# Kernel tuning notes

Hardware: AMD Instinct MI355X
Metric: run time of the kernel (lower is better)

## Reference

```python
import jax, jax.numpy as jnp
import numpy as np
import math

D, H, DK, F, V, L = 512, 8, 64, 2048, 8192, 2
B, S, T = 16, 128, 128
EPS = 1e-5


def _ln(x, g, b):
    mu = jnp.mean(x, -1, keepdims=True)
    var = jnp.mean((x - mu) ** 2, -1, keepdims=True)
    return g * (x - mu) * jax.lax.rsqrt(var + EPS) + b


def _pe(length):
    pos = jnp.arange(length, dtype=jnp.float32)[:, None]
    div = jnp.exp(jnp.arange(0, D, 2, dtype=jnp.float32) * (-math.log(10000.0) / D))
    ang = pos * div
    pe = jnp.zeros((length, D), jnp.float32)
    return pe.at[:, 0::2].set(jnp.sin(ang)).at[:, 1::2].set(jnp.cos(ang))


def _attn(q, k, v, src, dst, num_dst):
    # per-edge score = exp(clip((k_src . q_dst)/sqrt(d_k), -5, 5))  [E, H]
    score = jnp.einsum('ehd,ehd->eh', k[src], q[dst]) / math.sqrt(DK)
    score = jnp.exp(jnp.clip(score, -5.0, 5.0))
    wv = jax.ops.segment_sum(v[src] * score[..., None], dst, num_segments=num_dst)
    z = jax.ops.segment_sum(score, dst, num_segments=num_dst)
    return (wv / z[..., None]).reshape(num_dst, D)


def _forward(src_tokens, tgt_tokens, ee_src, ee_dst, dd_src, dd_dst, ed_src, ed_dst, P):
    (src_emb, tgt_emb, eW, eB, elg, elb, eW1, eb1, eW2, eb2, eng, enb,
     dsW, dsB, dcW, dcB, dlg, dlb, dW1, db1, dW2, db2, dng, dnb, gW, gb) = P
    pe = _pe(max(S, T))
    Ne, Nd = B * S, B * T
    xe = (src_emb[src_tokens] * math.sqrt(D) + pe[None, :S]).reshape(Ne, D)
    xd = (tgt_emb[tgt_tokens] * math.sqrt(D) + pe[None, :T]).reshape(Nd, D)
    # encoder stack
    for i in range(L):
        nx = _ln(xe, elg[i, 0], elb[i, 0])
        q = (nx @ eW[i, 0] + eB[i, 0]).reshape(Ne, H, DK)
        k = (nx @ eW[i, 1] + eB[i, 1]).reshape(Ne, H, DK)
        v = (nx @ eW[i, 2] + eB[i, 2]).reshape(Ne, H, DK)
        xe = xe + _attn(q, k, v, ee_src, ee_dst, Ne) @ eW[i, 3] + eB[i, 3]
        nx = _ln(xe, elg[i, 1], elb[i, 1])
        xe = xe + jax.nn.relu(nx @ eW1[i] + eb1[i]) @ eW2[i] + eb2[i]
        if i == L - 1:
            xe = _ln(xe, eng, enb)
    # decoder stack
    for i in range(L):
        nx = _ln(xd, dlg[i, 0], dlb[i, 0])
        q = (nx @ dsW[i, 0] + dsB[i, 0]).reshape(Nd, H, DK)
        k = (nx @ dsW[i, 1] + dsB[i, 1]).reshape(Nd, H, DK)
        v = (nx @ dsW[i, 2] + dsB[i, 2]).reshape(Nd, H, DK)
        xd = xd + _attn(q, k, v, dd_src, dd_dst, Nd) @ dsW[i, 3] + dsB[i, 3]
        nq = _ln(xd, dlg[i, 1], dlb[i, 1])
        nkv = _ln(xe, dlg[i, 1], dlb[i, 1])
        q = (nq @ dcW[i, 0] + dcB[i, 0]).reshape(Nd, H, DK)
        k = (nkv @ dcW[i, 1] + dcB[i, 1]).reshape(Ne, H, DK)
        v = (nkv @ dcW[i, 2] + dcB[i, 2]).reshape(Ne, H, DK)
        xd = xd + _attn(q, k, v, ed_src, ed_dst, Nd) @ dcW[i, 3] + dcB[i, 3]
        nx = _ln(xd, dlg[i, 2], dlb[i, 2])
        xd = xd + jax.nn.relu(nx @ dW1[i] + db1[i]) @ dW2[i] + db2[i]
        if i == L - 1:
            xd = _ln(xd, dng, dnb)
    return jax.nn.log_softmax(xd @ gW + gb, axis=-1)  # [Nd, V]


def setup_inputs() -> dict:
    key = jax.random.key(0)
    ks = iter(jax.random.split(key, 40))
    def nrm(shape, scale=0.02):
        return jax.random.normal(next(ks), shape, dtype=jnp.float32) * scale
    src_tokens = jax.random.randint(next(ks), (B, S), 0, V, dtype=jnp.int32)
    tgt_tokens = jax.random.randint(next(ks), (B, T), 0, V, dtype=jnp.int32)
    # graph structure (per-sentence blocks)
    si, di = np.meshgrid(np.arange(S), np.arange(S), indexing='ij')
    si, di = si.ravel(), di.ravel()
    base = (np.arange(B) * S)[:, None]
    ee_src = (base + si[None, :]).ravel().astype(np.int32)
    ee_dst = (base + di[None, :]).ravel().astype(np.int32)
    m = si <= di  # causal: src pos <= dst pos
    dd_src = (base + si[m][None, :]).ravel().astype(np.int32)
    dd_dst = (base + di[m][None, :]).ravel().astype(np.int32)
    ed_src = ee_src.copy()
    ed_dst = ee_dst.copy()
    inp = dict(
        src_tokens=src_tokens, tgt_tokens=tgt_tokens,
        ee_src=jnp.asarray(ee_src), ee_dst=jnp.asarray(ee_dst),
        dd_src=jnp.asarray(dd_src), dd_dst=jnp.asarray(dd_dst),
        ed_src=jnp.asarray(ed_src), ed_dst=jnp.asarray(ed_dst),
        src_emb=nrm((V, D), 1.0 / math.sqrt(D)), tgt_emb=nrm((V, D), 1.0 / math.sqrt(D)),
        enc_attn_W=nrm((L, 4, D, D)), enc_attn_b=jnp.zeros((L, 4, D), jnp.float32),
        enc_ln_g=jnp.ones((L, 2, D), jnp.float32), enc_ln_b=jnp.zeros((L, 2, D), jnp.float32),
        enc_ff_W1=nrm((L, D, F)), enc_ff_b1=jnp.zeros((L, F), jnp.float32),
        enc_ff_W2=nrm((L, F, D)), enc_ff_b2=jnp.zeros((L, D), jnp.float32),
        enc_norm_g=jnp.ones((D,), jnp.float32), enc_norm_b=jnp.zeros((D,), jnp.float32),
        dec_self_W=nrm((L, 4, D, D)), dec_self_b=jnp.zeros((L, 4, D), jnp.float32),
        dec_cross_W=nrm((L, 4, D, D)), dec_cross_b=jnp.zeros((L, 4, D), jnp.float32),
        dec_ln_g=jnp.ones((L, 3, D), jnp.float32), dec_ln_b=jnp.zeros((L, 3, D), jnp.float32),
        dec_ff_W1=nrm((L, D, F)), dec_ff_b1=jnp.zeros((L, F), jnp.float32),
        dec_ff_W2=nrm((L, F, D)), dec_ff_b2=jnp.zeros((L, D), jnp.float32),
        dec_norm_g=jnp.ones((D,), jnp.float32), dec_norm_b=jnp.zeros((D,), jnp.float32),
        gen_W=nrm((D, V)), gen_b=jnp.zeros((V,), jnp.float32),
    )
    return inp


def reference(src_tokens, tgt_tokens, ee_src, ee_dst, dd_src, dd_dst, ed_src, ed_dst,
              src_emb, tgt_emb, enc_attn_W, enc_attn_b, enc_ln_g, enc_ln_b,
              enc_ff_W1, enc_ff_b1, enc_ff_W2, enc_ff_b2, enc_norm_g, enc_norm_b,
              dec_self_W, dec_self_b, dec_cross_W, dec_cross_b, dec_ln_g, dec_ln_b,
              dec_ff_W1, dec_ff_b1, dec_ff_W2, dec_ff_b2, dec_norm_g, dec_norm_b,
              gen_W, gen_b):
    P = (src_emb, tgt_emb, enc_attn_W, enc_attn_b, enc_ln_g, enc_ln_b,
         enc_ff_W1, enc_ff_b1, enc_ff_W2, enc_ff_b2, enc_norm_g, enc_norm_b,
         dec_self_W, dec_self_b, dec_cross_W, dec_cross_b, dec_ln_g, dec_ln_b,
         dec_ff_W1, dec_ff_b1, dec_ff_W2, dec_ff_b2, dec_norm_g, dec_norm_b, gen_W, gen_b)
    return _forward(src_tokens, tgt_tokens, ee_src, ee_dst, dd_src, dd_dst, ed_src, ed_dst, P)
```

## Files before the change

### kernel.cpp

```cpp
#include <hip/hip_runtime.h>

typedef __attribute__((ext_vector_type(8))) short bfx8;
typedef __attribute__((ext_vector_type(4))) float fx4;

static __device__ __forceinline__ unsigned short f2bf(float f) {
    union { float f; unsigned int u; } v; v.f = f;
    unsigned int i = v.u;
    return (unsigned short)((i + 0x7FFFu + ((i >> 16) & 1u)) >> 16);
}
static __device__ __forceinline__ float bf2f(unsigned short u) {
    union { unsigned int ui; float f; } cv;
    cv.ui = ((unsigned int)u) << 16;
    return cv.f;
}

static __device__ __forceinline__ void gl2lds16(const unsigned short* g, unsigned short* l) {
    unsigned long long gu = (unsigned long long)g;
    unsigned int lu = (unsigned int)(unsigned long long)l;
    __builtin_amdgcn_global_load_lds(
        (const __attribute__((address_space(1))) void*)gu,
        (__attribute__((address_space(3))) void*)lu,
        16, 0, 0);
}

struct TrGroup {
    const float* src;
    unsigned short* dst;
    int srcRowStride;
    int dstRowStride;
    long srcSliceOff;
    long dstSliceOff;
};
struct TrTable {
    TrGroup g[18];
    int zStart[19];
};

__global__ __launch_bounds__(256) void trall_kernel(TrTable tt)
{
    __shared__ unsigned short tile[32][33];
    int z = blockIdx.z;
    int gi = 0;
#pragma unroll 1
    while (z >= tt.zStart[gi + 1]) ++gi;
    int zi = z - tt.zStart[gi];
    const float* s = tt.g[gi].src + (size_t)zi * tt.g[gi].srcSliceOff;
    unsigned short* d = tt.g[gi].dst + (size_t)zi * tt.g[gi].dstSliceOff;
    int srs = tt.g[gi].srcRowStride, drs = tt.g[gi].dstRowStride;
    int n0 = blockIdx.x * 32, k0 = blockIdx.y * 32;
    int tx = threadIdx.x & 31, ty = threadIdx.x >> 5;
#pragma unroll
    for (int i = 0; i < 32; i += 8)
        tile[ty + i][tx] = f2bf(s[(size_t)(k0 + ty + i) * srs + (n0 + tx)]);
    __syncthreads();
#pragma unroll
    for (int i = 0; i < 32; i += 8)
        d[(size_t)(n0 + ty + i) * drs + (k0 + tx)] = tile[tx][ty + i];
}

__global__ __launch_bounds__(256) void embed2_kernel(
    const int* __restrict__ tokA, const int* __restrict__ tokB,
    const float* __restrict__ embA, const float* __restrict__ embB,
    float* __restrict__ outA, float* __restrict__ outB)
{
    int idx = blockIdx.x;
    int row = idx & 2047;
    const int* tok = idx < 2048 ? tokA : tokB;
    const float* emb = idx < 2048 ? embA : embB;
    float* out = idx < 2048 ? outA : outB;
    int pos = row & 127;
    int t = tok[row];
    for (int d = threadIdx.x; d < 512; d += 256) {
        float ang = (float)pos * expf((float)(d & ~1) * (-9.210340371976184f / 512.0f));
        float pe = (d & 1) ? cosf(ang) : sinf(ang);
        out[(size_t)row * 512 + d] = emb[(size_t)t * 512 + d] * 22.627416997969522f + pe;
    }
}

static __device__ __forceinline__ void ln_row(
    const float* __restrict__ xrow, const float* __restrict__ g,
    const float* __restrict__ b, int lane, fx4& o0, fx4& o1)
{
    const fx4* xr = (const fx4*)xrow;
    fx4 a = xr[lane * 2], c = xr[lane * 2 + 1];
    float s = a[0] + a[1] + a[2] + a[3] + c[0] + c[1] + c[2] + c[3];
#pragma unroll
    for (int off = 32; off; off >>= 1) s += __shfl_xor(s, off);
    float mu = s * (1.0f / 512.0f);
    float qv = 0.f;
#pragma unroll
    for (int j = 0; j < 4; ++j) {
        float d0 = a[j] - mu; qv += d0 * d0;
        float d1 = c[j] - mu; qv += d1 * d1;
    }
#pragma unroll
    for (int off = 32; off; off >>= 1) qv += __shfl_xor(qv, off);
    float rs = rsqrtf(qv * (1.0f / 512.0f) + 1e-5f);
    const fx4* gr = (const fx4*)g;
    const fx4* br = (const fx4*)b;
    fx4 g0 = gr[lane * 2], g1 = gr[lane * 2 + 1];
    fx4 b0 = br[lane * 2], b1 = br[lane * 2 + 1];
#pragma unroll
    for (int j = 0; j < 4; ++j) {
        o0[j] = g0[j] * (a[j] - mu) * rs + b0[j];
        o1[j] = g1[j] * (c[j] - mu) * rs + b1[j];
    }
}

template<bool OUTBF>
__global__ __launch_bounds__(256) void ln_kernel(
    const float* __restrict__ x, const float* __restrict__ g,
    const float* __restrict__ b, void* __restrict__ out)
{
    int row = blockIdx.x * 4 + (threadIdx.x >> 6);
    int lane = threadIdx.x & 63;
    fx4 o0, o1;
    ln_row(x + (size_t)row * 512, g, b, lane, o0, o1);
    if (OUTBF) {
        unsigned short* orow = (unsigned short*)out + (size_t)row * 512 + lane * 8;
        ushort4 u0 = {f2bf(o0[0]), f2bf(o0[1]), f2bf(o0[2]), f2bf(o0[3])};
        ushort4 u1 = {f2bf(o1[0]), f2bf(o1[1]), f2bf(o1[2]), f2bf(o1[3])};
        *(ushort4*)orow = u0;
        *(ushort4*)(orow + 4) = u1;
    } else {
        fx4* orow = (fx4*)out + (size_t)row * 128;
        orow[lane * 2] = o0;
        orow[lane * 2 + 1] = o1;
    }
}

__global__ __launch_bounds__(256) void ln2_kernel(
    const float* __restrict__ x0, const float* __restrict__ x1,
    const float* __restrict__ g, const float* __restrict__ b,
    unsigned short* __restrict__ o0, unsigned short* __restrict__ o1)
{
    int idx = blockIdx.x * 4 + (threadIdx.x >> 6);
    int lane = threadIdx.x & 63;
    const float* x = idx < 2048 ? x0 : x1;
    unsigned short* o = idx < 2048 ? o0 : o1;
    int row = idx & 2047;
    fx4 v0, v1;
    ln_row(x + (size_t)row * 512, g, b, lane, v0, v1);
    unsigned short* orow = o + (size_t)row * 512 + lane * 8;
    ushort4 u0 = {f2bf(v0[0]), f2bf(v0[1]), f2bf(v0[2]), f2bf(v0[3])};
    ushort4 u1 = {f2bf(v1[0]), f2bf(v1[1]), f2bf(v1[2]), f2bf(v1[3])};
    *(ushort4*)orow = u0;
    *(ushort4*)(orow + 4) = u1;
}

template<bool RELU, bool RESID, bool OUTBF>
__global__ __launch_bounds__(256) void gemm_kernel(
    const unsigned short* __restrict__ A, const unsigned short* __restrict__ Wt,
    const float* __restrict__ bias, const float* __restrict__ res,
    void* __restrict__ Cv, int K, int ldc, int gx)
{
    __shared__ unsigned short smem[2][2][4096];
    const int tid = threadIdx.x;
    const int nwg = gridDim.x;
    const int cpx = nwg >> 3;
    const int phys = blockIdx.x;
    const int logical = (phys & 7) * cpx + (phys >> 3);
    const int bm = (logical / gx) * 64;
    const int bn = (logical % gx) * 64;
    const int lane = tid & 63;
    const int wv = tid >> 6;
    const int wr = (wv >> 1) * 32;
    const int wc = (wv & 1) * 32;
    const int lr = lane & 15;
    const int lrow = lane >> 3;
    const int lchk = lane & 7;
    fx4 acc00 = {0.f, 0.f, 0.f, 0.f}, acc01 = {0.f, 0.f, 0.f, 0.f};
    fx4 acc10 = {0.f, 0.f, 0.f, 0.f}, acc11 = {0.f, 0.f, 0.f, 0.f};

    auto stage = [&](int buf, int k0) {
#pragma unroll
        for (int j = 0; j < 2; ++j) {
            int row = wv * 16 + j * 8 + lrow;
            int sc = lchk ^ (row & 7);
            gl2lds16(A + (size_t)(bm + row) * K + k0 + sc * 8,
                     &smem[buf][0][(wv * 16 + j * 8) * 64]);
        }
#pragma unroll
        for (int j = 0; j < 2; ++j) {
            int row = wv * 16 + j * 8 + lrow;
            int sc = lchk ^ (row & 7);
            gl2lds16(Wt + (size_t)(bn + row) * K + k0 + sc * 8,
                     &smem[buf][1][(wv * 16 + j * 8) * 64]);
        }
    };

    const int nt = K >> 6;
    int cur = 0;
    stage(0, 0);
    for (int t = 0; t < nt; ++t) {
        __syncthreads();
        if (t + 1 < nt) stage(cur ^ 1, (t + 1) << 6);
        const unsigned short* bufA = &smem[cur][0][0];
        const unsigned short* bufB = &smem[cur][1][0];
        const int ra0 = wr + lr, ra1 = wr + 16 + lr;
        const int rb0 = wc + lr, rb1 = wc + 16 + lr;
#pragma unroll
        for (int kk = 0; kk < 2; ++kk) {
            int ca = kk * 4 + (lane >> 4);
            bfx8 a0 = *(const bfx8*)&bufA[ra0 * 64 + ((ca ^ (ra0 & 7)) * 8)];
            bfx8 a1 = *(const bfx8*)&bufA[ra1 * 64 + ((ca ^ (ra1 & 7)) * 8)];
            bfx8 b0 = *(const bfx8*)&bufB[rb0 * 64 + ((ca ^ (rb0 & 7)) * 8)];
            bfx8 b1 = *(const bfx8*)&bufB[rb1 * 64 + ((ca ^ (rb1 & 7)) * 8)];
            acc00 = __builtin_amdgcn_mfma_f32_16x16x32_bf16(a0, b0, acc00, 0, 0, 0);
            acc01 = __builtin_amdgcn_mfma_f32_16x16x32_bf16(a0, b1, acc01, 0, 0, 0);
            acc10 = __builtin_amdgcn_mfma_f32_16x16x32_bf16(a1, b0, acc10, 0, 0, 0);
            acc11 = __builtin_amdgcn_mfma_f32_16x16x32_bf16(a1, b1, acc11, 0, 0, 0);
        }
        cur ^= 1;
    }
    int rbase = bm + wr + ((lane >> 4) * 4);
    int cbase = bn + wc + lr;
#pragma unroll
    for (int m = 0; m < 2; ++m) {
        fx4 am0 = m ? acc10 : acc00;
        fx4 am1 = m ? acc11 : acc01;
#pragma unroll
        for (int r = 0; r < 4; ++r) {
            int row = rbase + m * 16 + r;
#pragma unroll
            for (int half = 0; half < 2; ++half) {
                int col = cbase + half * 16;
                float v = (half ? am1[r] : am0[r]) + bias[col];
                if (RESID) v += res[(size_t)row * ldc + col];
                if (RELU) v = fmaxf(v, 0.f);
                if (OUTBF) ((unsigned short*)Cv)[(size_t)row * ldc + col] = f2bf(v);
                else       ((float*)Cv)[(size_t)row * ldc + col] = v;
            }
        }
    }
}

template<bool RELU, bool RESID, bool OUTBF>
__global__ __launch_bounds__(256) void gemm_bk128_kernel(
    const unsigned short* __restrict__ A, const unsigned short* __restrict__ Wt,
    const float* __restrict__ bias, const float* __restrict__ res,
    void* __restrict__ Cv, int K, int ldc, int gx)
{
    __shared__ unsigned short smem[2][2][8192];
    const int tid = threadIdx.x;
    const int nwg = gridDim.x;
    const int cpx = nwg >> 3;
    const int phys = blockIdx.x;
    const int logical = (phys & 7) * cpx + (phys >> 3);
    const int bm = (logical / gx) * 64;
    const int bn = (logical % gx) * 64;
    const int lane = tid & 63;
    const int wv = tid >> 6;
    const int wr = (wv >> 1) * 32;
    const int wc = (wv & 1) * 32;
    const int lr = lane & 15;
    const int lrow4 = lane >> 4;
    const int lchk16 = lane & 15;
    fx4 acc00 = {0.f, 0.f, 0.f, 0.f}, acc01 = {0.f, 0.f, 0.f, 0.f};
    fx4 acc10 = {0.f, 0.f, 0.f, 0.f}, acc11 = {0.f, 0.f, 0.f, 0.f};

    auto stage = [&](int buf, int k0) {
#pragma unroll
        for (int j = 0; j < 4; ++j) {
            int row = wv * 16 + j * 4 + lrow4;
            int sc = (lchk16 ^ (row & 15)) * 8;
            gl2lds16(A + (size_t)(bm + row) * K + k0 + sc,
                     &smem[buf][0][(wv * 16 + j * 4) * 128]);
            gl2lds16(Wt + (size_t)(bn + row) * K + k0 + sc,
                     &smem[buf][1][(wv * 16 + j * 4) * 128]);
        }
    };

    const int nt = K >> 7;
    int cur = 0;
    stage(0, 0);
    for (int t = 0; t < nt; ++t) {
        __syncthreads();
        if (t + 1 < nt) stage(cur ^ 1, (t + 1) << 7);
        const unsigned short* bufA = &smem[cur][0][0];
        const unsigned short* bufB = &smem[cur][1][0];
        const int ra0 = wr + lr, ra1 = wr + 16 + lr;
        const int rb0 = wc + lr, rb1 = wc + 16 + lr;
#pragma unroll
        for (int kk = 0; kk < 4; ++kk) {
            int ca = kk * 4 + (lane >> 4);
            bfx8 a0 = *(const bfx8*)&bufA[ra0 * 128 + ((ca ^ (ra0 & 15)) * 8)];
            bfx8 a1 = *(const bfx8*)&bufA[ra1 * 128 + ((ca ^ (ra1 & 15)) * 8)];
            bfx8 b0 = *(const bfx8*)&bufB[rb0 * 128 + ((ca ^ (rb0 & 15)) * 8)];
            bfx8 b1 = *(const bfx8*)&bufB[rb1 * 128 + ((ca ^ (rb1 & 15)) * 8)];
            acc00 = __builtin_amdgcn_mfma_f32_16x16x32_bf16(a0, b0, acc00, 0, 0, 0);
            acc01 = __builtin_amdgcn_mfma_f32_16x16x32_bf16(a0, b1, acc01, 0, 0, 0);
            acc10 = __builtin_amdgcn_mfma_f32_16x16x32_bf16(a1, b0, acc10, 0, 0, 0);
            acc11 = __builtin_amdgcn_mfma_f32_16x16x32_bf16(a1, b1, acc11, 0, 0, 0);
        }
        cur ^= 1;
    }
    int rbase = bm + wr + ((lane >> 4) * 4);
    int cbase = bn + wc + lr;
#pragma unroll
    for (int m = 0; m < 2; ++m) {
        fx4 am0 = m ? acc10 : acc00;
        fx4 am1 = m ? acc11 : acc01;
#pragma unroll
        for (int r = 0; r < 4; ++r) {
            int row = rbase + m * 16 + r;
#pragma unroll
            for (int half = 0; half < 2; ++half) {
                int col = cbase + half * 16;
                float v = (half ? am1[r] : am0[r]) + bias[col];
                if (RESID) v += res[(size_t)row * ldc + col];
                if (RELU) v = fmaxf(v, 0.f);
                if (OUTBF) ((unsigned short*)Cv)[(size_t)row * ldc + col] = f2bf(v);
                else       ((float*)Cv)[(size_t)row * ldc + col] = v;
            }
        }
    }
}

template<bool RELU>
__global__ __launch_bounds__(256) void gemm128_kernel(
    const unsigned short* __restrict__ A, const unsigned short* __restrict__ Wt,
    const float* __restrict__ bias, unsigned short* __restrict__ C,
    int K, int ldc)
{
    __shared__ unsigned short smem[2][2][8192];
    const int tid = threadIdx.x;
    const int nwg = gridDim.x;
    const int cpx = nwg >> 3;
    const int phys = blockIdx.x;
    const int logical = (phys & 7) * cpx + (phys >> 3);
    const int bm = (logical & 15) * 128;
    const int bn = (logical >> 4) * 128;
    const int lane = tid & 63;
    const int wv = tid >> 6;
    const int wr = (wv >> 1) * 64;
    const int wc = (wv & 1) * 64;
    const int lr = lane & 15;
    const int lrow = lane >> 3;
    const int lchk = lane & 7;
    fx4 acc[4][4];
#pragma unroll
    for (int mi = 0; mi < 4; ++mi)
#pragma unroll
        for (int ni = 0; ni < 4; ++ni) acc[mi][ni] = fx4{0.f, 0.f, 0.f, 0.f};

    auto stage = [&](int buf, int k0) {
#pragma unroll
        for (int j = 0; j < 4; ++j) {
            int row = wv * 32 + j * 8 + lrow;
            int sc = lchk ^ (row & 7);
            gl2lds16(A + (size_t)(bm + row) * K + k0 + sc * 8,
                     &smem[buf][0][(wv * 32 + j * 8) * 64]);
            gl2lds16(Wt + (size_t)(bn + row) * K + k0 + sc * 8,
                     &smem[buf][1][(wv * 32 + j * 8) * 64]);
        }
    };

    const int nt = K >> 6;
    int cur = 0;
    stage(0, 0);
    for (int t = 0; t < nt; ++t) {
        __syncthreads();
        if (t + 1 < nt) stage(cur ^ 1, (t + 1) << 6);
        const unsigned short* bufA = &smem[cur][0][0];
        const unsigned short* bufB = &smem[cur][1][0];
#pragma unroll
        for (int kk = 0; kk < 2; ++kk) {
            int ca = kk * 4 + (lane >> 4);
            bfx8 af[4], bg[4];
#pragma unroll
            for (int i = 0; i < 4; ++i) {
                int ra = wr + i * 16 + lr;
                int rb = wc + i * 16 + lr;
                af[i] = *(const bfx8*)&bufA[ra * 64 + ((ca ^ (ra & 7)) * 8)];
                bg[i] = *(const bfx8*)&bufB[rb * 64 + ((ca ^ (rb & 7)) * 8)];
            }
#pragma unroll
            for (int mi = 0; mi < 4; ++mi)
#pragma unroll
                for (int ni = 0; ni < 4; ++ni)
                    acc[mi][ni] = __builtin_amdgcn_mfma_f32_16x16x32_bf16(af[mi], bg[ni], acc[mi][ni], 0, 0, 0);
        }
        cur ^= 1;
    }
    int rbase = bm + wr + ((lane >> 4) * 4);
    int cbase = bn + wc + lr;
#pragma unroll
    for (int mi = 0; mi < 4; ++mi)
#pragma unroll
        for (int ni = 0; ni < 4; ++ni) {
            int col = cbase + ni * 16;
            float bv = bias[col];
#pragma unroll
            for (int r = 0; r < 4; ++r) {
                int row = rbase + mi * 16 + r;
                float v = acc[mi][ni][r] + bv;
                if (RELU) v = fmaxf(v, 0.f);
                C[(size_t)row * ldc + col] = f2bf(v);
            }
        }
}

template<bool CAUSAL>
__global__ __launch_bounds__(512) void fattn_kernel(
    const unsigned short* __restrict__ xq, const unsigned short* __restrict__ xkv,
    const unsigned short* __restrict__ Wt, const float* __restrict__ bias,
    unsigned short* __restrict__ out)
{
    __shared__ __align__(16) unsigned char lds[143872];
    const int blk = blockIdx.x;
    const int half = blk & 1;
    const int h = (blk >> 1) & 7;
    const int b = blk >> 4;
    const int q0 = half * 64;
    const int tid = threadIdx.x;
    const int lane = tid & 63;
    const int wv = tid >> 6;
    const int lr = lane & 15;
    const int hg8 = (lane >> 4) * 8;
    const int rloc = (lane >> 4) * 4;
    const int lrow = lane >> 3;
    const int lchk = lane & 7;

    const unsigned short* gxq = xq + (size_t)(b * 128 + q0) * 512;
    const unsigned short* gkv = xkv + (size_t)(b * 128) * 512;
    const unsigned short* gw  = Wt + (size_t)(h * 64) * 512;

    auto stage = [&](int buf, int k0) {
        unsigned short* dstX = (unsigned short*)(lds + buf * 49152);
        unsigned short* dstW = (unsigned short*)(lds + buf * 49152 + 24576);
#pragma unroll
        for (int j = 0; j < 3; ++j) {
            int row = wv * 24 + j * 8 + lrow;
            int sc = (lchk ^ (row & 7)) * 8;
            const unsigned short* xs = (row < 64)
                ? gxq + (size_t)row * 512
                : gkv + (size_t)(row - 64) * 512;
            gl2lds16(xs + k0 + sc, dstX + (wv * 24 + j * 8) * 64);
            const unsigned short* ws = gw + ((size_t)(row & 63) + (size_t)(row >> 6) * 512) * 512;
            gl2lds16(ws + k0 + sc, dstW + (wv * 24 + j * 8) * 64);
        }
    };

    fx4 accQ[4], accK[4], accV[4];
#pragma unroll
    for (int c = 0; c < 4; ++c) {
        accQ[c] = fx4{0.f, 0.f, 0.f, 0.f};
        accK[c] = fx4{0.f, 0.f, 0.f, 0.f};
        accV[c] = fx4{0.f, 0.f, 0.f, 0.f};
    }
    stage(0, 0);
#pragma unroll 1
    for (int t = 0; t < 8; ++t) {
        __syncthreads();
        if (t < 7) stage((t + 1) & 1, (t + 1) * 64);
        const unsigned short* stX = (const unsigned short*)(lds + (t & 1) * 49152);
        const unsigned short* stW = (const unsigned short*)(lds + (t & 1) * 49152 + 24576);
#pragma unroll
        for (int kk = 0; kk < 2; ++kk) {
            const int ca = kk * 4 + (lane >> 4);
            auto rd = [&](const unsigned short* base, int row) -> bfx8 {
                return *(const bfx8*)(base + row * 64 + ((ca ^ (row & 7)) * 8));
            };
            bfx8 aKV = rd(stX, 64 + wv * 16 + lr);
            bfx8 aQ = aKV;
            if (wv >= 4) aQ = rd(stX, (wv - 4) * 16 + lr);
#pragma unroll
            for (int c = 0; c < 4; ++c) {
                bfx8 bk = rd(stW, 64 + c * 16 + lr);
                accK[c] = __builtin_amdgcn_mfma_f32_16x16x32_bf16(aKV, bk, accK[c], 0, 0, 0);
                bfx8 bv = rd(stW, 128 + c * 16 + lr);
                accV[c] = __builtin_amdgcn_mfma_f32_16x16x32_bf16(aKV, bv, accV[c], 0, 0, 0);
                if (wv >= 4) {
                    bfx8 bq = rd(stW, c * 16 + lr);
                    accQ[c] = __builtin_amdgcn_mfma_f32_16x16x32_bf16(aQ, bq, accQ[c], 0, 0, 0);
                }
            }
        }
    }
    unsigned short* sQ  = (unsigned short*)(lds + 98304);
    unsigned short* sK  = (unsigned short*)(lds + 107520);
    unsigned short* sVt = (unsigned short*)(lds + 125952);
    float* zp = (float*)(lds + 143360);
    unsigned short* sP  = (unsigned short*)lds;
#pragma unroll
    for (int c = 0; c < 4; ++c) {
        int col = c * 16 + lr;
        float bk_ = bias[512 + h * 64 + col];
        float bv_ = bias[1024 + h * 64 + col];
#pragma unroll
        for (int r = 0; r < 4; ++r) {
            sK[(wv * 16 + rloc + r) * 72 + col] = f2bf(accK[c][r] + bk_);
            sVt[col * 136 + (wv * 16 + rloc + r)] = f2bf(accV[c][r] + bv_);
        }
        if (wv >= 4) {
            float bq_ = bias[h * 64 + col];
#pragma unroll
            for (int r = 0; r < 4; ++r)
                sQ[((wv - 4) * 16 + rloc + r) * 72 + col] = f2bf(accQ[c][r] + bq_);
        }
    }
    __syncthreads();
    const int qb = wv >> 1;
    const int kh = wv & 1;
    fx4 acc[4];
#pragma unroll
    for (int n = 0; n < 4; ++n) acc[n] = fx4{0.f, 0.f, 0.f, 0.f};
#pragma unroll
    for (int kk = 0; kk < 2; ++kk) {
        bfx8 a = *(const bfx8*)(sQ + (qb * 16 + lr) * 72 + kk * 32 + hg8);
#pragma unroll
        for (int n = 0; n < 4; ++n) {
            bfx8 bb = *(const bfx8*)(sK + ((kh * 4 + n) * 16 + lr) * 72 + kk * 32 + hg8);
            acc[n] = __builtin_amdgcn_mfma_f32_16x16x32_bf16(a, bb, acc[n], 0, 0, 0);
        }
    }
    const int qg = q0 + qb * 16 + rloc;
#pragma unroll
    for (int r = 0; r < 4; ++r) {
        float zs = 0.f;
#pragma unroll
        for (int n = 0; n < 4; ++n) {
            float s = acc[n][r] * 0.125f;
            s = __expf(fminf(fmaxf(s, -5.f), 5.f));
            if (CAUSAL && (kh * 64 + n * 16 + lr) > (qg + r)) s = 0.f;
            zs += s;
            sP[(qb * 16 + rloc + r) * 136 + kh * 64 + n * 16 + lr] = f2bf(s);
        }
#pragma unroll
        for (int off = 8; off; off >>= 1) zs += __shfl_xor(zs, off);
        if (lr == 0) zp[(qb * 2 + kh) * 16 + rloc + r] = zs;
    }
    __syncthreads();
    float zinv[4];
#pragma unroll
    for (int r = 0; r < 4; ++r)
        zinv[r] = 1.f / (zp[(qb * 2 + 0) * 16 + rloc + r] + zp[(qb * 2 + 1) * 16 + rloc + r]);
    const int dh = wv & 1;
    fx4 acc2[2];
    acc2[0] = fx4{0.f, 0.f, 0.f, 0.f};
    acc2[1] = fx4{0.f, 0.f, 0.f, 0.f};
#pragma unroll
    for (int kk = 0; kk < 4; ++kk) {
        bfx8 a = *(const bfx8*)(sP + (qb * 16 + lr) * 136 + kk * 32 + hg8);
#pragma unroll
        for (int dn = 0; dn < 2; ++dn) {
            bfx8 bb = *(const bfx8*)(sVt + (dh * 32 + dn * 16 + lr) * 136 + kk * 32 + hg8);
            acc2[dn] = __builtin_amdgcn_mfma_f32_16x16x32_bf16(a, bb, acc2[dn], 0, 0, 0);
        }
    }
#pragma unroll
    for (int dn = 0; dn < 2; ++dn)
#pragma unroll
        for (int r = 0; r < 4; ++r) {
            size_t row = (size_t)(b * 128 + qg + r);
            out[row * 512 + h * 64 + dh * 32 + dn * 16 + lr] = f2bf(acc2[dn][r] * zinv[r]);
        }
}

__global__ __launch_bounds__(256) void logsoftmax_bf16_kernel(
    const unsigned short* __restrict__ logits, float* __restrict__ out)
{
    __shared__ float red[4];
    int tid = threadIdx.x;
    const bfx8* lrow = (const bfx8*)(logits + (size_t)blockIdx.x * 8192);
    float* orow = out + (size_t)blockIdx.x * 8192;
    float vals[32];
    float mx = -1e30f;
#pragma unroll
    for (int i = 0; i < 4; ++i) {
        bfx8 u = lrow[i * 256 + tid];
#pragma unroll
        for (int j = 0; j < 8; ++j) {
            float f = bf2f((unsigned short)u[j]);
            vals[i * 8 + j] = f;
            mx = fmaxf(mx, f);
        }
    }
#pragma unroll
    for (int off = 32; off; off >>= 1) mx = fmaxf(mx, __shfl_xor(mx, off));
    int wid = tid >> 6;
    if ((tid & 63) == 0) red[wid] = mx;
    __syncthreads();
    mx = fmaxf(fmaxf(red[0], red[1]), fmaxf(red[2], red[3]));
    __syncthreads();
    float sum = 0.f;
#pragma unroll
    for (int i = 0; i < 32; ++i) sum += __expf(vals[i] - mx);
#pragma unroll
    for (int off = 32; off; off >>= 1) sum += __shfl_xor(sum, off);
    if ((tid & 63) == 0) red[wid] = sum;
    __syncthreads();
    sum = red[0] + red[1] + red[2] + red[3];
    float lsub = mx + logf(sum);
#pragma unroll
    for (int i = 0; i < 4; ++i) {
        fx4 o0, o1;
#pragma unroll
        for (int j = 0; j < 4; ++j) {
            o0[j] = vals[i * 8 + j] - lsub;
            o1[j] = vals[i * 8 + 4 + j] - lsub;
        }
        ((fx4*)orow)[(i * 256 + tid) * 2] = o0;
        ((fx4*)orow)[(i * 256 + tid) * 2 + 1] = o1;
    }
}

extern "C" void kernel_launch(void* const* d_in, const int* in_sizes, int n_in,
                              void* d_out, int out_size, void* d_ws, size_t ws_size,
                              hipStream_t stream) {
    (void)in_sizes; (void)n_in; (void)out_size; (void)ws_size;
    const int* src_tokens = (const int*)d_in[0];
    const int* tgt_tokens = (const int*)d_in[1];
    const float* src_emb    = (const float*)d_in[8];
    const float* tgt_emb    = (const float*)d_in[9];
    const float* enc_attn_W = (const float*)d_in[10];
    const float* enc_attn_b = (const float*)d_in[11];
    const float* enc_ln_g   = (const float*)d_in[12];
    const float* enc_ln_b   = (const float*)d_in[13];
    const float* enc_ff_W1  = (const float*)d_in[14];
    const float* enc_ff_b1  = (const float*)d_in[15];
    const float* enc_ff_W2  = (const float*)d_in[16];
    const float* enc_ff_b2  = (const float*)d_in[17];
    const float* enc_norm_g = (const float*)d_in[18];
    const float* enc_norm_b = (const float*)d_in[19];
    const float* dec_self_W = (const float*)d_in[20];
    const float* dec_self_b = (const float*)d_in[21];
    const float* dec_cross_W= (const float*)d_in[22];
    const float* dec_cross_b= (const float*)d_in[23];
    const float* dec_ln_g   = (const float*)d_in[24];
    const float* dec_ln_b   = (const float*)d_in[25];
    const float* dec_ff_W1  = (const float*)d_in[26];
    const float* dec_ff_b1  = (const float*)d_in[27];
    const float* dec_ff_W2  = (const float*)d_in[28];
    const float* dec_ff_b2  = (const float*)d_in[29];
    const float* dec_norm_g = (const float*)d_in[30];
    const float* dec_norm_b = (const float*)d_in[31];
    const float* gen_W      = (const float*)d_in[32];
    const float* gen_b      = (const float*)d_in[33];
    float* dout = (float*)d_out;

    unsigned short* wt = (unsigned short*)d_ws;
    const size_t OFF_ENCQKV = 0;
    const size_t OFF_ENCO   = 1572864;
    const size_t OFF_ENCW1  = 2097152;
    const size_t OFF_ENCW2  = 4194304;
    const size_t OFF_DECSQKV= 6291456;
    const size_t OFF_DECSO  = 7864320;
    const size_t OFF_DECCQKV= 8388608;
    const size_t OFF_DECCO  = 9961472;
    const size_t OFF_DECW1  = 10485760;
    const size_t OFF_DECW2  = 12582912;
    const size_t OFF_GENW   = 14680064;
    const size_t WT_ELEMS   = 18874368;
    float* fb  = (float*)(wt + WT_ELEMS);
    float* xe  = fb;
    float* xd  = fb + 1048576;
    unsigned short* nxb  = (unsigned short*)(fb + 2097152);
    unsigned short* nkvb = (unsigned short*)(fb + 3145728);
    unsigned short* ffb  = (unsigned short*)(fb + 4194304);
    unsigned short* attb = (unsigned short*)(fb + 7340032);
    unsigned short* genin   = (unsigned short*)fb;
    unsigned short* logitsb = (unsigned short*)(fb + 1048576);

    TrTable tt;
    {
        int z = 0, gi = 0;
        auto addg = [&](const float* s, unsigned short* d, int srs, int drs,
                        long so, long dof, int zc) {
            tt.zStart[gi] = z;
            tt.g[gi].src = s; tt.g[gi].dst = d;
            tt.g[gi].srcRowStride = srs; tt.g[gi].dstRowStride = drs;
            tt.g[gi].srcSliceOff = so; tt.g[gi].dstSliceOff = dof;
            ++gi; z += zc;
        };
        addg(enc_attn_W,              wt + OFF_ENCQKV,               512,  512,  262144,    262144, 3);
        addg(enc_attn_W + 4L*262144,  wt + OFF_ENCQKV + 3L*262144,   512,  512,  262144,    262144, 3);
        addg(enc_attn_W + 3L*262144,  wt + OFF_ENCO,                 512,  512,  4L*262144, 262144, 2);
        addg(enc_ff_W1,               wt + OFF_ENCW1,                2048, 512,  512,       262144, 4);
        addg(enc_ff_W1 + 1048576,     wt + OFF_ENCW1 + 1048576,      2048, 512,  512,       262144, 4);
        addg(enc_ff_W2,               wt + OFF_ENCW2,                512,  2048, 262144,    512,    4);
        addg(enc_ff_W2 + 1048576,     wt + OFF_ENCW2 + 1048576,      512,  2048, 262144,    512,    4);
        addg(dec_self_W,              wt + OFF_DECSQKV,              512,  512,  262144,    262144, 3);
        addg(dec_self_W + 4L*262144,  wt + OFF_DECSQKV + 3L*262144,  512,  512,  262144,    262144, 3);
        addg(dec_self_W + 3L*262144,  wt + OFF_DECSO,                512,  512,  4L*262144, 262144, 2);
        addg(dec_cross_W,             wt + OFF_DECCQKV,              512,  512,  262144,    262144, 3);
        addg(dec_cross_W + 4L*262144, wt + OFF_DECCQKV + 3L*262144,  512,  512,  262144,    262144, 3);
        addg(dec_cross_W + 3L*262144, wt + OFF_DECCO,                512,  512,  4L*262144, 262144, 2);
        addg(dec_ff_W1,               wt + OFF_DECW1,                2048, 512,  512,       262144, 4);
        addg(dec_ff_W1 + 1048576,     wt + OFF_DECW1 + 1048576,      2048, 512,  512,       262144, 4);
        addg(dec_ff_W2,               wt + OFF_DECW2,                512,  2048, 262144,    512,    4);
        addg(dec_ff_W2 + 1048576,     wt + OFF_DECW2 + 1048576,      512,  2048, 262144,    512,    4);
        addg(gen_W,                   wt + OFF_GENW,                 8192, 512,  512,       262144, 16);
        tt.zStart[18] = z;
    }
    trall_kernel<<<dim3(16, 16, 72), 256, 0, stream>>>(tt);

    embed2_kernel<<<4096, 256, 0, stream>>>(src_tokens, tgt_tokens, src_emb, tgt_emb, xe, xd);

    auto gemm = [&](const unsigned short* A, const unsigned short* W, const float* bias,
                    const float* res, void* C, int N, int K, int ldc, bool relu, bool outbf) {
        int gx = N / 64;
        dim3 g(gx * 32);
        if (res)        gemm_kernel<false, true,  false><<<g, 256, 0, stream>>>(A, W, bias, res, C, K, ldc, gx);
        else if (relu)  gemm_kernel<true,  false, true ><<<g, 256, 0, stream>>>(A, W, bias, res, C, K, ldc, gx);
        else if (outbf) gemm_kernel<false, false, true ><<<g, 256, 0, stream>>>(A, W, bias, res, C, K, ldc, gx);
        else            gemm_kernel<false, false, false><<<g, 256, 0, stream>>>(A, W, bias, res, C, K, ldc, gx);
    };
    auto gemmK128res = [&](const unsigned short* A, const unsigned short* W, const float* bias,
                           const float* res, float* C, int N, int K, int ldc) {
        int gx = N / 64;
        dim3 g(gx * 32);
        gemm_bk128_kernel<false, true, false><<<g, 256, 0, stream>>>(A, W, bias, res, C, K, ldc, gx);
    };
    auto gemm128 = [&](const unsigned short* A, const unsigned short* W, const float* bias,
                       unsigned short* C, int N, int K, int ldc, bool relu) {
        dim3 g((N / 128) * 16);
        if (relu) gemm128_kernel<true ><<<g, 256, 0, stream>>>(A, W, bias, C, K, ldc);
        else      gemm128_kernel<false><<<g, 256, 0, stream>>>(A, W, bias, C, K, ldc);
    };
    auto lnb = [&](const float* x, const float* g, const float* b, unsigned short* o) {
        ln_kernel<true><<<512, 256, 0, stream>>>(x, g, b, o);
    };
    auto lnf = [&](const float* x, const float* g, const float* b, float* o) {
        ln_kernel<false><<<512, 256, 0, stream>>>(x, g, b, o);
    };

    for (int i = 0; i < 2; ++i) {
        lnb(xe, enc_ln_g + (size_t)(i * 2 + 0) * 512, enc_ln_b + (size_t)(i * 2 + 0) * 512, nxb);
        fattn_kernel<false><<<256, 512, 0, stream>>>(
            nxb, nxb, wt + OFF_ENCQKV + (size_t)i * 3 * 262144,
            enc_attn_b + (size_t)i * 4 * 512, attb);
        gemm(attb, wt + OFF_ENCO + (size_t)i * 262144, enc_attn_b + (size_t)i * 4 * 512 + 1536,
             xe, xe, 512, 512, 512, false, false);
        lnb(xe, enc_ln_g + (size_t)(i * 2 + 1) * 512, enc_ln_b + (size_t)(i * 2 + 1) * 512, nxb);
        gemm128(nxb, wt + OFF_ENCW1 + (size_t)i * 1048576, enc_ff_b1 + (size_t)i * 2048,
                ffb, 2048, 512, 2048, true);
        gemmK128res(ffb, wt + OFF_ENCW2 + (size_t)i * 1048576, enc_ff_b2 + (size_t)i * 512,
                    xe, xe, 512, 2048, 512);
    }
    lnf(xe, enc_norm_g, enc_norm_b, xe);

    for (int i = 0; i < 2; ++i) {
        lnb(xd, dec_ln_g + (size_t)(i * 3 + 0) * 512, dec_ln_b + (size_t)(i * 3 + 0) * 512, nxb);
        fattn_kernel<true><<<256, 512, 0, stream>>>(
            nxb, nxb, wt + OFF_DECSQKV + (size_t)i * 3 * 262144,
            dec_self_b + (size_t)i * 4 * 512, attb);
        gemm(attb, wt + OFF_DECSO + (size_t)i * 262144, dec_self_b + (size_t)i * 4 * 512 + 1536,
             xd, xd, 512, 512, 512, false, false);
        ln2_kernel<<<1024, 256, 0, stream>>>(
            xd, xe, dec_ln_g + (size_t)(i * 3 + 1) * 512, dec_ln_b + (size_t)(i * 3 + 1) * 512,
            nxb, nkvb);
        fattn_kernel<false><<<256, 512, 0, stream>>>(
            nxb, nkvb, wt + OFF_DECCQKV + (size_t)i * 3 * 262144,
            dec_cross_b + (size_t)i * 4 * 512, attb);
        gemm(attb, wt + OFF_DECCO + (size_t)i * 262144, dec_cross_b + (size_t)i * 4 * 512 + 1536,
             xd, xd, 512, 512, 512, false, false);
        lnb(xd, dec_ln_g + (size_t)(i * 3 + 2) * 512, dec_ln_b + (size_t)(i * 3 + 2) * 512, nxb);
        gemm128(nxb, wt + OFF_DECW1 + (size_t)i * 1048576, dec_ff_b1 + (size_t)i * 2048,
                ffb, 2048, 512, 2048, true);
        gemmK128res(ffb, wt + OFF_DECW2 + (size_t)i * 1048576, dec_ff_b2 + (size_t)i * 512,
                    xd, xd, 512, 2048, 512);
    }
    lnb(xd, dec_norm_g, dec_norm_b, genin);

    gemm128(genin, wt + OFF_GENW, gen_b, logitsb, 8192, 512, 8192, false);
    logsoftmax_bf16_kernel<<<2048, 256, 0, stream>>>(logitsb, dout);
}
```

Measured before the change: 342.0 us.

## Specialize self-attention staging, add MFMA priority hints, unify GEMMs on BK128

Adds a SELF template flag to the fused attention kernel. When q and kv are the same tensor, it stages 128 shared X rows once instead of loading the 64 query rows separately, which reduces LDS footprint and global loads per tile. Wraps MFMA inner loops in s_setprio(1)/s_setprio(0) so compute waves get scheduling priority over loads. Removes the BK64 GEMM kernel and routes all N=512 projections through the BK128 variant, which halves loop iterations for K=512 but uses more LDS per block.

```diff
diff --git a/kernel.cpp b/kernel.cpp
--- a/kernel.cpp
+++ b/kernel.cpp
@@ -146,93 +146,6 @@
     ushort4 u1 = {f2bf(v1[0]), f2bf(v1[1]), f2bf(v1[2]), f2bf(v1[3])};
     *(ushort4*)orow = u0;
     *(ushort4*)(orow + 4) = u1;
-}
-
-template<bool RELU, bool RESID, bool OUTBF>
-__global__ __launch_bounds__(256) void gemm_kernel(
-    const unsigned short* __restrict__ A, const unsigned short* __restrict__ Wt,
-    const float* __restrict__ bias, const float* __restrict__ res,
-    void* __restrict__ Cv, int K, int ldc, int gx)
-{
-    __shared__ unsigned short smem[2][2][4096];
-    const int tid = threadIdx.x;
-    const int nwg = gridDim.x;
-    const int cpx = nwg >> 3;
-    const int phys = blockIdx.x;
-    const int logical = (phys & 7) * cpx + (phys >> 3);
-    const int bm = (logical / gx) * 64;
-    const int bn = (logical % gx) * 64;
-    const int lane = tid & 63;
-    const int wv = tid >> 6;
-    const int wr = (wv >> 1) * 32;
-    const int wc = (wv & 1) * 32;
-    const int lr = lane & 15;
-    const int lrow = lane >> 3;
-    const int lchk = lane & 7;
-    fx4 acc00 = {0.f, 0.f, 0.f, 0.f}, acc01 = {0.f, 0.f, 0.f, 0.f};
-    fx4 acc10 = {0.f, 0.f, 0.f, 0.f}, acc11 = {0.f, 0.f, 0.f, 0.f};
-
-    auto stage = [&](int buf, int k0) {
-#pragma unroll
-        for (int j = 0; j < 2; ++j) {
-            int row = wv * 16 + j * 8 + lrow;
-            int sc = lchk ^ (row & 7);
-            gl2lds16(A + (size_t)(bm + row) * K + k0 + sc * 8,
-                     &smem[buf][0][(wv * 16 + j * 8) * 64]);
-        }
-#pragma unroll
-        for (int j = 0; j < 2; ++j) {
-            int row = wv * 16 + j * 8 + lrow;
-            int sc = lchk ^ (row & 7);
-            gl2lds16(Wt + (size_t)(bn + row) * K + k0 + sc * 8,
-                     &smem[buf][1][(wv * 16 + j * 8) * 64]);
-        }
-    };
-
-    const int nt = K >> 6;
-    int cur = 0;
-    stage(0, 0);
-    for (int t = 0; t < nt; ++t) {
-        __syncthreads();
-        if (t + 1 < nt) stage(cur ^ 1, (t + 1) << 6);
-        const unsigned short* bufA = &smem[cur][0][0];
-        const unsigned short* bufB = &smem[cur][1][0];
-        const int ra0 = wr + lr, ra1 = wr + 16 + lr;
-        const int rb0 = wc + lr, rb1 = wc + 16 + lr;
-#pragma unroll
-        for (int kk = 0; kk < 2; ++kk) {
-            int ca = kk * 4 + (lane >> 4);
-            bfx8 a0 = *(const bfx8*)&bufA[ra0 * 64 + ((ca ^ (ra0 & 7)) * 8)];
-            bfx8 a1 = *(const bfx8*)&bufA[ra1 * 64 + ((ca ^ (ra1 & 7)) * 8)];
-            bfx8 b0 = *(const bfx8*)&bufB[rb0 * 64 + ((ca ^ (rb0 & 7)) * 8)];
-            bfx8 b1 = *(const bfx8*)&bufB[rb1 * 64 + ((ca ^ (rb1 & 7)) * 8)];
-            acc00 = __builtin_amdgcn_mfma_f32_16x16x32_bf16(a0, b0, acc00, 0, 0, 0);
-            acc01 = __builtin_amdgcn_mfma_f32_16x16x32_bf16(a0, b1, acc01, 0, 0, 0);
-            acc10 = __builtin_amdgcn_mfma_f32_16x16x32_bf16(a1, b0, acc10, 0, 0, 0);
-            acc11 = __builtin_amdgcn_mfma_f32_16x16x32_bf16(a1, b1, acc11, 0, 0, 0);
-        }
-        cur ^= 1;
-    }
-    int rbase = bm + wr + ((lane >> 4) * 4);
-    int cbase = bn + wc + lr;
-#pragma unroll
-    for (int m = 0; m < 2; ++m) {
-        fx4 am0 = m ? acc10 : acc00;
-        fx4 am1 = m ? acc11 : acc01;
-#pragma unroll
-        for (int r = 0; r < 4; ++r) {
-            int row = rbase + m * 16 + r;
-#pragma unroll
-            for (int half = 0; half < 2; ++half) {
-                int col = cbase + half * 16;
-                float v = (half ? am1[r] : am0[r]) + bias[col];
-                if (RESID) v += res[(size_t)row * ldc + col];
-                if (RELU) v = fmaxf(v, 0.f);
-                if (OUTBF) ((unsigned short*)Cv)[(size_t)row * ldc + col] = f2bf(v);
-                else       ((float*)Cv)[(size_t)row * ldc + col] = v;
-            }
-        }
-    }
 }
 
 template<bool RELU, bool RESID, bool OUTBF>
@@ -281,6 +194,7 @@
         const unsigned short* bufB = &smem[cur][1][0];
         const int ra0 = wr + lr, ra1 = wr + 16 + lr;
         const int rb0 = wc + lr, rb1 = wc + 16 + lr;
+        __builtin_amdgcn_s_setprio(1);
 #pragma unroll
         for (int kk = 0; kk < 4; ++kk) {
             int ca = kk * 4 + (lane >> 4);
@@ -293,6 +207,7 @@
             acc10 = __builtin_amdgcn_mfma_f32_16x16x32_bf16(a1, b0, acc10, 0, 0, 0);
             acc11 = __builtin_amdgcn_mfma_f32_16x16x32_bf16(a1, b1, acc11, 0, 0, 0);
         }
+        __builtin_amdgcn_s_setprio(0);
         cur ^= 1;
     }
     int rbase = bm + wr + ((lane >> 4) * 4);
@@ -364,6 +279,7 @@
         if (t + 1 < nt) stage(cur ^ 1, (t + 1) << 6);
         const unsigned short* bufA = &smem[cur][0][0];
         const unsigned short* bufB = &smem[cur][1][0];
+        __builtin_amdgcn_s_setprio(1);
 #pragma unroll
         for (int kk = 0; kk < 2; ++kk) {
             int ca = kk * 4 + (lane >> 4);
@@ -381,6 +297,7 @@
                 for (int ni = 0; ni < 4; ++ni)
                     acc[mi][ni] = __builtin_amdgcn_mfma_f32_16x16x32_bf16(af[mi], bg[ni], acc[mi][ni], 0, 0, 0);
         }
+        __builtin_amdgcn_s_setprio(0);
         cur ^= 1;
     }
     int rbase = bm + wr + ((lane >> 4) * 4);
@@ -401,13 +318,15 @@
         }
 }
 
-template<bool CAUSAL>
+template<bool CAUSAL, bool SELF>
 __global__ __launch_bounds__(512) void fattn_kernel(
     const unsigned short* __restrict__ xq, const unsigned short* __restrict__ xkv,
     const unsigned short* __restrict__ Wt, const float* __restrict__ bias,
     unsigned short* __restrict__ out)
 {
-    __shared__ __align__(16) unsigned char lds[143872];
+    constexpr int XROWS = SELF ? 128 : 192;
+    constexpr int BUFB  = (XROWS + 192) * 64 * 2;
+    __shared__ __align__(16) unsigned char lds[2 * BUFB + 9216 + 18432 + 17408 + 512];
     const int blk = blockIdx.x;
     const int half = blk & 1;
     const int h = (blk >> 1) & 7;
@@ -427,18 +346,35 @@
     const unsigned short* gw  = Wt + (size_t)(h * 64) * 512;
 
     auto stage = [&](int buf, int k0) {
-        unsigned short* dstX = (unsigned short*)(lds + buf * 49152);
-        unsigned short* dstW = (unsigned short*)(lds + buf * 49152 + 24576);
-#pragma unroll
-        for (int j = 0; j < 3; ++j) {
-            int row = wv * 24 + j * 8 + lrow;
-            int sc = (lchk ^ (row & 7)) * 8;
-            const unsigned short* xs = (row < 64)
-                ? gxq + (size_t)row * 512
-                : gkv + (size_t)(row - 64) * 512;
-            gl2lds16(xs + k0 + sc, dstX + (wv * 24 + j * 8) * 64);
-            const unsigned short* ws = gw + ((size_t)(row & 63) + (size_t)(row >> 6) * 512) * 512;
-            gl2lds16(ws + k0 + sc, dstW + (wv * 24 + j * 8) * 64);
+        unsigned short* dst = (unsigned short*)(lds + buf * BUFB);
+        if constexpr (SELF) {
+#pragma unroll
+            for (int j = 0; j < 5; ++j) {
+                int start = wv * 40 + j * 8;
+                int row = start + lrow;
+                int sc = (lchk ^ (row & 7)) * 8;
+                const unsigned short* src;
+                if (start < 128) {
+                    src = gkv + (size_t)row * 512 + k0 + sc;
+                } else {
+                    int wr_ = row - 128;
+                    src = gw + ((size_t)(wr_ & 63) + (size_t)(wr_ >> 6) * 512) * 512 + k0 + sc;
+                }
+                gl2lds16(src, dst + start * 64);
+            }
+        } else {
+            unsigned short* dstW = dst + XROWS * 64;
+#pragma unroll
+            for (int j = 0; j < 3; ++j) {
+                int row = wv * 24 + j * 8 + lrow;
+                int sc = (lchk ^ (row & 7)) * 8;
+                const unsigned short* xs = (row < 64)
+                    ? gxq + (size_t)row * 512
+                    : gkv + (size_t)(row - 64) * 512;
+                gl2lds16(xs + k0 + sc, dst + (wv * 24 + j * 8) * 64);
+                const unsigned short* ws = gw + ((size_t)(row & 63) + (size_t)(row >> 6) * 512) * 512;
+                gl2lds16(ws + k0 + sc, dstW + (wv * 24 + j * 8) * 64);
+            }
         }
     };
 
@@ -454,17 +390,19 @@
     for (int t = 0; t < 8; ++t) {
         __syncthreads();
         if (t < 7) stage((t + 1) & 1, (t + 1) * 64);
-        const unsigned short* stX = (const unsigned short*)(lds + (t & 1) * 49152);
-        const unsigned short* stW = (const unsigned short*)(lds + (t & 1) * 49152 + 24576);
+        const unsigned short* stX = (const unsigned short*)(lds + (t & 1) * BUFB);
+        const unsigned short* stW = stX + XROWS * 64;
 #pragma unroll
         for (int kk = 0; kk < 2; ++kk) {
             const int ca = kk * 4 + (lane >> 4);
             auto rd = [&](const unsigned short* base, int row) -> bfx8 {
                 return *(const bfx8*)(base + row * 64 + ((ca ^ (row & 7)) * 8));
             };
-            bfx8 aKV = rd(stX, 64 + wv * 16 + lr);
+            const int kvbase = SELF ? 0 : 64;
+            bfx8 aKV = rd(stX, kvbase + wv * 16 + lr);
             bfx8 aQ = aKV;
-            if (wv >= 4) aQ = rd(stX, (wv - 4) * 16 + lr);
+            if (wv >= 4) aQ = rd(stX, (SELF ? q0 : 0) + (wv - 4) * 16 + lr);
+            __builtin_amdgcn_s_setprio(1);
 #pragma unroll
             for (int c = 0; c < 4; ++c) {
                 bfx8 bk = rd(stW, 64 + c * 16 + lr);
@@ -476,12 +414,13 @@
                     accQ[c] = __builtin_amdgcn_mfma_f32_16x16x32_bf16(aQ, bq, accQ[c], 0, 0, 0);
                 }
             }
-        }
-    }
-    unsigned short* sQ  = (unsigned short*)(lds + 98304);
-    unsigned short* sK  = (unsigned short*)(lds + 107520);
-    unsigned short* sVt = (unsigned short*)(lds + 125952);
-    float* zp = (float*)(lds + 143360);
+            __builtin_amdgcn_s_setprio(0);
+        }
+    }
+    unsigned short* sQ  = (unsigned short*)(lds + 2 * BUFB);
+    unsigned short* sK  = (unsigned short*)(lds + 2 * BUFB + 9216);
+    unsigned short* sVt = (unsigned short*)(lds + 2 * BUFB + 9216 + 18432);
+    float* zp = (float*)(lds + 2 * BUFB + 9216 + 18432 + 17408);
     unsigned short* sP  = (unsigned short*)lds;
 #pragma unroll
     for (int c = 0; c < 4; ++c) {
@@ -698,20 +637,14 @@
 
     embed2_kernel<<<4096, 256, 0, stream>>>(src_tokens, tgt_tokens, src_emb, tgt_emb, xe, xd);
 
-    auto gemm = [&](const unsigned short* A, const unsigned short* W, const float* bias,
-                    const float* res, void* C, int N, int K, int ldc, bool relu, bool outbf) {
+    auto gemmK = [&](const unsigned short* A, const unsigned short* W, const float* bias,
+                     const float* res, void* C, int N, int K, int ldc, bool relu, bool outbf) {
         int gx = N / 64;
         dim3 g(gx * 32);
-        if (res)        gemm_kernel<false, true,  false><<<g, 256, 0, stream>>>(A, W, bias, res, C, K, ldc, gx);
-        else if (relu)  gemm_kernel<true,  false, true ><<<g, 256, 0, stream>>>(A, W, bias, res, C, K, ldc, gx);
-        else if (outbf) gemm_kernel<false, false, true ><<<g, 256, 0, stream>>>(A, W, bias, res, C, K, ldc, gx);
-        else            gemm_kernel<false, false, false><<<g, 256, 0, stream>>>(A, W, bias, res, C, K, ldc, gx);
-    };
-    auto gemmK128res = [&](const unsigned short* A, const unsigned short* W, const float* bias,
-                           const float* res, float* C, int N, int K, int ldc) {
-        int gx = N / 64;
-        dim3 g(gx * 32);
-        gemm_bk128_kernel<false, true, false><<<g, 256, 0, stream>>>(A, W, bias, res, C, K, ldc, gx);
+        if (res)        gemm_bk128_kernel<false, true,  false><<<g, 256, 0, stream>>>(A, W, bias, res, C, K, ldc, gx);
+        else if (relu)  gemm_bk128_kernel<true,  false, true ><<<g, 256, 0, stream>>>(A, W, bias, res, C, K, ldc, gx);
+        else if (outbf) gemm_bk128_kernel<false, false, true ><<<g, 256, 0, stream>>>(A, W, bias, res, C, K, ldc, gx);
+        else            gemm_bk128_kernel<false, false, false><<<g, 256, 0, stream>>>(A, W, bias, res, C, K, ldc, gx);
     };
     auto gemm128 = [&](const unsigned short* A, const unsigned short* W, const float* bias,
                        unsigned short* C, int N, int K, int ldc, bool relu) {
@@ -728,39 +661,39 @@
 
     for (int i = 0; i < 2; ++i) {
         lnb(xe, enc_ln_g + (size_t)(i * 2 + 0) * 512, enc_ln_b + (size_t)(i * 2 + 0) * 512, nxb);
-        fattn_kernel<false><<<256, 512, 0, stream>>>(
+        fattn_kernel<false, true><<<256, 512, 0, stream>>>(
             nxb, nxb, wt + OFF_ENCQKV + (size_t)i * 3 * 262144,
             enc_attn_b + (size_t)i * 4 * 512, attb);
-        gemm(attb, wt + OFF_ENCO + (size_t)i * 262144, enc_attn_b + (size_t)i * 4 * 512 + 1536,
-             xe, xe, 512, 512, 512, false, false);
+        gemmK(attb, wt + OFF_ENCO + (size_t)i * 262144, enc_attn_b + (size_t)i * 4 * 512 + 1536,
+              xe, xe, 512, 512, 512, false, false);
         lnb(xe, enc_ln_g + (size_t)(i * 2 + 1) * 512, enc_ln_b + (size_t)(i * 2 + 1) * 512, nxb);
         gemm128(nxb, wt + OFF_ENCW1 + (size_t)i * 1048576, enc_ff_b1 + (size_t)i * 2048,
                 ffb, 2048, 512, 2048, true);
-        gemmK128res(ffb, wt + OFF_ENCW2 + (size_t)i * 1048576, enc_ff_b2 + (size_t)i * 512,
-                    xe, xe, 512, 2048, 512);
+        gemmK(ffb, wt + OFF_ENCW2 + (size_t)i * 1048576, enc_ff_b2 + (size_t)i * 512,
+              xe, xe, 512, 2048, 512, false, false);
     }
     lnf(xe, enc_norm_g, enc_norm_b, xe);
 
     for (int i = 0; i < 2; ++i) {
         lnb(xd, dec_ln_g + (size_t)(i * 3 + 0) * 512, dec_ln_b + (size_t)(i * 3 + 0) * 512, nxb);
-        fattn_kernel<true><<<256, 512, 0, stream>>>(
+        fattn_kernel<true, true><<<256, 512, 0, stream>>>(
             nxb, nxb, wt + OFF_DECSQKV + (size_t)i * 3 * 262144,
             dec_self_b + (size_t)i * 4 * 512, attb);
-        gemm(attb, wt + OFF_DECSO + (size_t)i * 262144, dec_self_b + (size_t)i * 4 * 512 + 1536,
-             xd, xd, 512, 512, 512, false, false);
+        gemmK(attb, wt + OFF_DECSO + (size_t)i * 262144, dec_self_b + (size_t)i * 4 * 512 + 1536,
+              xd, xd, 512, 512, 512, false, false);
         ln2_kernel<<<1024, 256, 0, stream>>>(
             xd, xe, dec_ln_g + (size_t)(i * 3 + 1) * 512, dec_ln_b + (size_t)(i * 3 + 1) * 512,
             nxb, nkvb);
-        fattn_kernel<false><<<256, 512, 0, stream>>>(
+        fattn_kernel<false, false><<<256, 512, 0, stream>>>(
             nxb, nkvb, wt + OFF_DECCQKV + (size_t)i * 3 * 262144,
             dec_cross_b + (size_t)i * 4 * 512, attb);
-        gemm(attb, wt + OFF_DECCO + (size_t)i * 262144, dec_cross_b + (size_t)i * 4 * 512 + 1536,
-             xd, xd, 512, 512, 512, false, false);
+        gemmK(attb, wt + OFF_DECCO + (size_t)i * 262144, dec_cross_b + (size_t)i * 4 * 512 + 1536,
+              xd, xd, 512, 512, 512, false, false);
         lnb(xd, dec_ln_g + (size_t)(i * 3 + 2) * 512, dec_ln_b + (size_t)(i * 3 + 2) * 512, nxb);
         gemm128(nxb, wt + OFF_DECW1 + (size_t)i * 1048576, dec_ff_b1 + (size_t)i * 2048,
                 ffb, 2048, 512, 2048, true);
-        gemmK128res(ffb, wt + OFF_DECW2 + (size_t)i * 1048576, dec_ff_b2 + (size_t)i * 512,
-                    xd, xd, 512, 2048, 512);
+        gemmK(ffb, wt + OFF_DECW2 + (size_t)i * 1048576, dec_ff_b2 + (size_t)i * 512,
+              xd, xd, 512, 2048, 512, false, false);
     }
     lnb(xd, dec_norm_g, dec_norm_b, genin);
 
```

Measured after the change: 336.7 us. Within noise of the previous version (-1.5%).
